# Kernel tuning notes

Hardware: AMD Instinct MI355X
Metric: run time of the kernel (lower is better)

The kernel has to match this reference:

```python
import jax, jax.numpy as jnp
import numpy as np

B, W, F = 64, 128, 64          # batch, window (node feat dim), n_features (nodes)
H, OUTW = 4, 128               # num_heads, out window size
NEG_SLOPE = 0.2                # LeakyReLU negative slope (alpha)


def setup_inputs() -> dict:
    key = jax.random.key(0)
    ks = jax.random.split(key, 6)
    scale_in = 1.0 / np.sqrt(W)
    scale_a = 1.0 / np.sqrt(OUTW)
    return {
        "x": jax.random.normal(ks[0], (B, W, F), dtype=jnp.float32),
        "W_src": jax.random.normal(ks[1], (H * OUTW, W), dtype=jnp.float32) * scale_in,
        "b_src": jnp.zeros((H * OUTW,), dtype=jnp.float32),
        "W_dst": jax.random.normal(ks[2], (H * OUTW, W), dtype=jnp.float32) * scale_in,
        "b_dst": jnp.zeros((H * OUTW,), dtype=jnp.float32),
        "attn": jax.random.normal(ks[3], (H, OUTW), dtype=jnp.float32) * scale_a,
    }


def reference(x, W_src, b_src, W_dst, b_dst, attn):
    # x: [B, W, F] -> node features nf: [B, F, W] (F nodes, W-dim features)
    nf = jnp.transpose(x, (0, 2, 1))
    b, f, w = nf.shape
    h, outw = attn.shape
    # GATv2 separate source/destination projections (share_weights=False)
    fs = (nf @ W_src.T + b_src).reshape(b, f, h, outw)  # [B, F, H, outW]
    fd = (nf @ W_dst.T + b_dst).reshape(b, f, h, outw)
    # additive score over complete graph with self-loops: e[b,i,j,h,d]
    s = fs[:, :, None, :, :] + fd[:, None, :, :, :]      # [B, src, dst, H, outW]
    e = jnp.where(s >= 0, s, NEG_SLOPE * s)              # LeakyReLU
    scores = jnp.einsum('bijhd,hd->bhij', e, attn)       # [B, H, src, dst]
    # edge softmax: normalize over incoming edges (sources) per destination
    a = jax.nn.softmax(scores, axis=2)
    # weighted scatter-sum aggregation at destinations
    out = jnp.einsum('bhij,bihd->bjhd', a, fs)           # [B, F, H, outW]
    out = out.mean(axis=2)                               # mean over heads -> [B, F, outW]
    return jnp.transpose(out, (0, 2, 1))                 # [B, outW, F]
```

## Files before the change

kernel.cpp:

```cpp
#include <hip/hip_runtime.h>
#include <math.h>

#define BB 64
#define WW 128
#define FF 64
#define HH 4
#define OW 128


struct GemmRegion {
    float xq[64 * 68];
    float wq[2 * 128 * 68];
};
struct AttnRegion {
    float fsl[FF * 132];
    float fdl[FF * 132];
    float st[FF * 68];
    float A6[OW], B4[OW];
    float redm[8 * 64];
    float reds[8 * 64];
};
union SMem { GemmRegion g; AttnRegion a; };

__global__ void __launch_bounds__(512)
__attribute__((amdgpu_waves_per_eu(2, 2)))
gat_fused(
    const float* __restrict__ x,
    const float* __restrict__ Wsrc,
    const float* __restrict__ bsrc,
    const float* __restrict__ Wdst,
    const float* __restrict__ bdst,
    const float* __restrict__ attn,
    float* __restrict__ out)
{
    __shared__ __align__(16) SMem sm;
    __shared__ float bl[2 * 128];

    const int bx = blockIdx.x;
    const int h  = bx & 3;
    const int b  = bx >> 2;
    const int t  = threadIdx.x;

    const int m  = t >> 7;
    const int ig = (t >> 4) & 7;
    const int dg = t & 15;
    const int i0 = ig * 8;

    if (t < 256) bl[t] = (t & 128 ? bdst : bsrc)[h * 128 + (t & 127)];

    float acc[8][8] = {};

    for (int kh = 0; kh < 2; ++kh) {
        if (kh) __syncthreads();
        #pragma unroll
        for (int p = 0; p < 2; ++p) {
            const int idx = p * 512 + t;
            const int k = idx >> 4, iq = idx & 15;
            *(float4*)&sm.g.xq[k * 68 + iq * 4] =
                *(const float4*)(x + ((size_t)b * WW + kh * 64 + k) * FF + iq * 4);
        }
        #pragma unroll
        for (int p = 0; p < 8; ++p) {
            const int idx = p * 512 + t;
            const int mm = idx >> 11, d = (idx >> 4) & 127, q = idx & 15;
            *(float4*)&sm.g.wq[(mm * 128 + d) * 68 + q * 4] =
                *(const float4*)((mm ? Wdst : Wsrc)
                                 + (size_t)(h * 128 + d) * WW + kh * 64 + q * 4);
        }
        __syncthreads();

        if (t < 256) {
            #pragma unroll 1
            for (int k0 = 0; k0 < 64; k0 += 4) {
                float4 wv[8];
                #pragma unroll
                for (int e = 0; e < 8; ++e)
                    wv[e] = *(const float4*)&sm.g.wq[(m * 128 + dg + 16 * e) * 68 + k0];
                #pragma unroll
                for (int kk = 0; kk < 4; ++kk) {
                    const float4 xa = *(const float4*)&sm.g.xq[(k0 + kk) * 68 + i0];
                    const float4 xb = *(const float4*)&sm.g.xq[(k0 + kk) * 68 + i0 + 4];
                    #pragma unroll
                    for (int e = 0; e < 8; ++e) {
                        const float wf = ((const float*)&wv[e])[kk];
                        acc[0][e] = fmaf(xa.x, wf, acc[0][e]);
                        acc[1][e] = fmaf(xa.y, wf, acc[1][e]);
                        acc[2][e] = fmaf(xa.z, wf, acc[2][e]);
                        acc[3][e] = fmaf(xa.w, wf, acc[3][e]);
                        acc[4][e] = fmaf(xb.x, wf, acc[4][e]);
                        acc[5][e] = fmaf(xb.y, wf, acc[5][e]);
                        acc[6][e] = fmaf(xb.z, wf, acc[6][e]);
                        acc[7][e] = fmaf(xb.w, wf, acc[7][e]);
                    }
                }
            }
        }
    }
    __syncthreads();

    if (t < 256) {
        float* dst = m ? sm.a.fdl : sm.a.fsl;
        #pragma unroll
        for (int e = 0; e < 8; ++e) {
            const int d = dg + 16 * e;
            const float bv = bl[m * 128 + d];
            #pragma unroll
            for (int ii = 0; ii < 8; ++ii)
                dst[(i0 + ii) * 132 + d] = acc[ii][e] + bv;
        }
    }
    if (t < 128) {
        const float av = attn[h * OW + t];
        sm.a.A6[t] = 0.6f * av;
        sm.a.B4[t] = 0.4f * av;
    }
    __syncthreads();

    if (t < 256) {
        const int i = t & 63, sel = t >> 6;
        const float* src = (sel < 2 ? sm.a.fsl : sm.a.fdl) + i * 132 + (sel & 1) * 64;
        const float* a6  = sm.a.A6 + (sel & 1) * 64;
        float s = 0.0f;
        #pragma unroll
        for (int c = 0; c < 16; ++c) {
            float4 fv = *(const float4*)&src[c * 4];
            float4 av = *(const float4*)&a6[c * 4];
            s = fmaf(fv.x, av.x, fmaf(fv.y, av.y, fmaf(fv.z, av.z, fmaf(fv.w, av.w, s))));
        }
        sm.a.redm[sel * 64 + i] = s;
    }
    __syncthreads();

    {
        const int lane = t & 63;
        const int jl0  = (t >> 6) * 8;
        float sc[8] = {};
        #pragma unroll 4
        for (int c = 0; c < 32; ++c) {
            const int dd0 = c * 4;
            float4 fsv = *(const float4*)&sm.a.fsl[lane * 132 + dd0];
            float4 b4  = *(const float4*)&sm.a.B4[dd0];
            #pragma unroll
            for (int jj = 0; jj < 8; ++jj) {
                float4 fdv = *(const float4*)&sm.a.fdl[(jl0 + jj) * 132 + dd0];
                float r = sc[jj];
                r = fmaf(b4.x, fabsf(fsv.x + fdv.x), r);
                r = fmaf(b4.y, fabsf(fsv.y + fdv.y), r);
                r = fmaf(b4.z, fabsf(fsv.z + fdv.z), r);
                r = fmaf(b4.w, fabsf(fsv.w + fdv.w), r);
                sc[jj] = r;
            }
        }
        const float csl = sm.a.redm[lane] + sm.a.redm[64 + lane];
        float4 o0, o1;
        o0.x = sc[0] + csl + sm.a.redm[128 + jl0 + 0] + sm.a.redm[192 + jl0 + 0];
        o0.y = sc[1] + csl + sm.a.redm[128 + jl0 + 1] + sm.a.redm[192 + jl0 + 1];
        o0.z = sc[2] + csl + sm.a.redm[128 + jl0 + 2] + sm.a.redm[192 + jl0 + 2];
        o0.w = sc[3] + csl + sm.a.redm[128 + jl0 + 3] + sm.a.redm[192 + jl0 + 3];
        o1.x = sc[4] + csl + sm.a.redm[128 + jl0 + 4] + sm.a.redm[192 + jl0 + 4];
        o1.y = sc[5] + csl + sm.a.redm[128 + jl0 + 5] + sm.a.redm[192 + jl0 + 5];
        o1.z = sc[6] + csl + sm.a.redm[128 + jl0 + 6] + sm.a.redm[192 + jl0 + 6];
        o1.w = sc[7] + csl + sm.a.redm[128 + jl0 + 7] + sm.a.redm[192 + jl0 + 7];
        *(float4*)&sm.a.st[lane * 68 + jl0]     = o0;
        *(float4*)&sm.a.st[lane * 68 + jl0 + 4] = o1;
    }
    __syncthreads();

    {
        const int j = t & 63, s = t >> 6;
        const int i0s = s * 8;
        float mx = sm.a.st[i0s * 68 + j];
        #pragma unroll
        for (int k = 1; k < 8; ++k) mx = fmaxf(mx, sm.a.st[(i0s + k) * 68 + j]);
        sm.a.redm[s * 64 + j] = mx;
    }
    __syncthreads();
    {
        const int j = t & 63, s = t >> 6;
        const int i0s = s * 8;
        float mj = sm.a.redm[j];
        #pragma unroll
        for (int s2 = 1; s2 < 8; ++s2) mj = fmaxf(mj, sm.a.redm[s2 * 64 + j]);
        float ps = 0.0f;
        #pragma unroll
        for (int k = 0; k < 8; ++k) {
            float e = __expf(sm.a.st[(i0s + k) * 68 + j] - mj);
            sm.a.st[(i0s + k) * 68 + j] = e;
            ps += e;
        }
        sm.a.reds[s * 64 + j] = ps;
    }
    __syncthreads();

    {
        const int j = t & 63, dblk = t >> 6;
        float l = 0.0f;
        #pragma unroll
        for (int s2 = 0; s2 < 8; ++s2) l += sm.a.reds[s2 * 64 + j];
        const float iv = 0.25f / l;

        float ag[16] = {};
        #pragma unroll 4
        for (int i = 0; i < FF; ++i) {
            const float p = sm.a.st[i * 68 + j];
            const float* fr = &sm.a.fsl[i * 132 + dblk * 16];
            float4 f0 = *(const float4*)(fr);
            float4 f1 = *(const float4*)(fr + 4);
            float4 f2 = *(const float4*)(fr + 8);
            float4 f3 = *(const float4*)(fr + 12);
            ag[0]  = fmaf(p, f0.x, ag[0]);  ag[1]  = fmaf(p, f0.y, ag[1]);
            ag[2]  = fmaf(p, f0.z, ag[2]);  ag[3]  = fmaf(p, f0.w, ag[3]);
            ag[4]  = fmaf(p, f1.x, ag[4]);  ag[5]  = fmaf(p, f1.y, ag[5]);
            ag[6]  = fmaf(p, f1.z, ag[6]);  ag[7]  = fmaf(p, f1.w, ag[7]);
            ag[8]  = fmaf(p, f2.x, ag[8]);  ag[9]  = fmaf(p, f2.y, ag[9]);
            ag[10] = fmaf(p, f2.z, ag[10]); ag[11] = fmaf(p, f2.w, ag[11]);
            ag[12] = fmaf(p, f3.x, ag[12]); ag[13] = fmaf(p, f3.y, ag[13]);
            ag[14] = fmaf(p, f3.z, ag[14]); ag[15] = fmaf(p, f3.w, ag[15]);
        }
        float* ob = out + ((size_t)b * OW + dblk * 16) * FF + j;
        #pragma unroll
        for (int e = 0; e < 16; ++e)
            atomicAdd(ob + e * FF, ag[e] * iv);
    }
}

extern "C" void kernel_launch(void* const* d_in, const int* in_sizes, int n_in,
                              void* d_out, int out_size, void* d_ws, size_t ws_size,
                              hipStream_t stream) {
    const float* x    = (const float*)d_in[0];
    const float* Wsrc = (const float*)d_in[1];
    const float* bsrc = (const float*)d_in[2];
    const float* Wdst = (const float*)d_in[3];
    const float* bdst = (const float*)d_in[4];
    const float* attn = (const float*)d_in[5];

    hipMemsetAsync(d_out, 0, (size_t)out_size, stream);
    gat_fused<<<BB * HH, 512, 0, stream>>>(x, Wsrc, bsrc, Wdst, bdst, attn,
                                           (float*)d_out);
}
```

Measured before the change: 105.2 us.

## Stream GEMM weights from global into registers and retile score and aggregation loops

```diff
diff --git a/kernel.cpp b/kernel.cpp
--- a/kernel.cpp
+++ b/kernel.cpp
@@ -10,12 +10,12 @@
 
 struct GemmRegion {
     float xq[64 * 68];
-    float wq[2 * 128 * 68];
 };
 struct AttnRegion {
     float fsl[FF * 132];
     float fdl[FF * 132];
     float st[FF * 68];
+    float st2[FF * 68];
     float A6[OW], B4[OW];
     float redm[8 * 64];
     float reds[8 * 64];
@@ -41,12 +41,14 @@
     const int b  = bx >> 2;
     const int t  = threadIdx.x;
 
-    const int m  = t >> 7;
+    const int m  = (t >> 7) & 1;
     const int ig = (t >> 4) & 7;
     const int dg = t & 15;
     const int i0 = ig * 8;
 
     if (t < 256) bl[t] = (t & 128 ? bdst : bsrc)[h * 128 + (t & 127)];
+
+    const float* wbase = (m ? Wdst : Wsrc) + (size_t)(h * 128 + dg) * WW;
 
     float acc[8][8] = {};
 
@@ -59,23 +61,22 @@
             *(float4*)&sm.g.xq[k * 68 + iq * 4] =
                 *(const float4*)(x + ((size_t)b * WW + kh * 64 + k) * FF + iq * 4);
         }
-        #pragma unroll
-        for (int p = 0; p < 8; ++p) {
-            const int idx = p * 512 + t;
-            const int mm = idx >> 11, d = (idx >> 4) & 127, q = idx & 15;
-            *(float4*)&sm.g.wq[(mm * 128 + d) * 68 + q * 4] =
-                *(const float4*)((mm ? Wdst : Wsrc)
-                                 + (size_t)(h * 128 + d) * WW + kh * 64 + q * 4);
-        }
         __syncthreads();
 
         if (t < 256) {
+            const float* wk = wbase + kh * 64;
+            float4 wv[8];
+            #pragma unroll
+            for (int e = 0; e < 8; ++e)
+                wv[e] = *(const float4*)(wk + (size_t)(16 * e) * WW);
             #pragma unroll 1
             for (int k0 = 0; k0 < 64; k0 += 4) {
-                float4 wv[8];
-                #pragma unroll
-                for (int e = 0; e < 8; ++e)
-                    wv[e] = *(const float4*)&sm.g.wq[(m * 128 + dg + 16 * e) * 68 + k0];
+                float4 wn[8];
+                if (k0 < 60) {
+                    #pragma unroll
+                    for (int e = 0; e < 8; ++e)
+                        wn[e] = *(const float4*)(wk + (size_t)(16 * e) * WW + k0 + 4);
+                }
                 #pragma unroll
                 for (int kk = 0; kk < 4; ++kk) {
                     const float4 xa = *(const float4*)&sm.g.xq[(k0 + kk) * 68 + i0];
@@ -93,6 +94,8 @@
                         acc[7][e] = fmaf(xb.w, wf, acc[7][e]);
                     }
                 }
+                #pragma unroll
+                for (int e = 0; e < 8; ++e) wv[e] = wn[e];
             }
         }
     }
@@ -132,37 +135,59 @@
     __syncthreads();
 
     {
-        const int lane = t & 63;
-        const int jl0  = (t >> 6) * 8;
-        float sc[8] = {};
+        const int dh  = t >> 8;
+        const int rem = t & 255;
+        const int i0D = (rem & 15) * 4;
+        const int j0D = (rem >> 4) * 4;
+        float4 scq[4];
+        scq[0] = scq[1] = scq[2] = scq[3] = float4{0.f, 0.f, 0.f, 0.f};
+        const int cBase = dh * 16;
         #pragma unroll 4
-        for (int c = 0; c < 32; ++c) {
-            const int dd0 = c * 4;
-            float4 fsv = *(const float4*)&sm.a.fsl[lane * 132 + dd0];
-            float4 b4  = *(const float4*)&sm.a.B4[dd0];
-            #pragma unroll
-            for (int jj = 0; jj < 8; ++jj) {
-                float4 fdv = *(const float4*)&sm.a.fdl[(jl0 + jj) * 132 + dd0];
-                float r = sc[jj];
-                r = fmaf(b4.x, fabsf(fsv.x + fdv.x), r);
-                r = fmaf(b4.y, fabsf(fsv.y + fdv.y), r);
-                r = fmaf(b4.z, fabsf(fsv.z + fdv.z), r);
-                r = fmaf(b4.w, fabsf(fsv.w + fdv.w), r);
-                sc[jj] = r;
-            }
-        }
-        const float csl = sm.a.redm[lane] + sm.a.redm[64 + lane];
-        float4 o0, o1;
-        o0.x = sc[0] + csl + sm.a.redm[128 + jl0 + 0] + sm.a.redm[192 + jl0 + 0];
-        o0.y = sc[1] + csl + sm.a.redm[128 + jl0 + 1] + sm.a.redm[192 + jl0 + 1];
-        o0.z = sc[2] + csl + sm.a.redm[128 + jl0 + 2] + sm.a.redm[192 + jl0 + 2];
-        o0.w = sc[3] + csl + sm.a.redm[128 + jl0 + 3] + sm.a.redm[192 + jl0 + 3];
-        o1.x = sc[4] + csl + sm.a.redm[128 + jl0 + 4] + sm.a.redm[192 + jl0 + 4];
-        o1.y = sc[5] + csl + sm.a.redm[128 + jl0 + 5] + sm.a.redm[192 + jl0 + 5];
-        o1.z = sc[6] + csl + sm.a.redm[128 + jl0 + 6] + sm.a.redm[192 + jl0 + 6];
-        o1.w = sc[7] + csl + sm.a.redm[128 + jl0 + 7] + sm.a.redm[192 + jl0 + 7];
-        *(float4*)&sm.a.st[lane * 68 + jl0]     = o0;
-        *(float4*)&sm.a.st[lane * 68 + jl0 + 4] = o1;
+        for (int c = 0; c < 16; ++c) {
+            const int dd0 = (cBase + c) * 4;
+            const float4 b4 = *(const float4*)&sm.a.B4[dd0];
+            float4 fdv[4];
+            #pragma unroll
+            for (int jj = 0; jj < 4; ++jj)
+                fdv[jj] = *(const float4*)&sm.a.fdl[(j0D + jj) * 132 + dd0];
+            #pragma unroll
+            for (int ii = 0; ii < 4; ++ii) {
+                const float4 fsv = *(const float4*)&sm.a.fsl[(i0D + ii) * 132 + dd0];
+                float* sc = (float*)&scq[ii];
+                #pragma unroll
+                for (int jj = 0; jj < 4; ++jj) {
+                    float r = sc[jj];
+                    r = fmaf(b4.x, fabsf(fsv.x + fdv[jj].x), r);
+                    r = fmaf(b4.y, fabsf(fsv.y + fdv[jj].y), r);
+                    r = fmaf(b4.z, fabsf(fsv.z + fdv[jj].z), r);
+                    r = fmaf(b4.w, fabsf(fsv.w + fdv[jj].w), r);
+                    sc[jj] = r;
+                }
+            }
+        }
+        if (dh) {
+            #pragma unroll
+            for (int ii = 0; ii < 4; ++ii)
+                *(float4*)&sm.a.st2[(i0D + ii) * 68 + j0D] = scq[ii];
+        }
+        __syncthreads();
+        if (!dh) {
+            float cdj[4];
+            #pragma unroll
+            for (int jj = 0; jj < 4; ++jj)
+                cdj[jj] = sm.a.redm[128 + j0D + jj] + sm.a.redm[192 + j0D + jj];
+            #pragma unroll
+            for (int ii = 0; ii < 4; ++ii) {
+                const float4 p2 = *(const float4*)&sm.a.st2[(i0D + ii) * 68 + j0D];
+                const float csl = sm.a.redm[i0D + ii] + sm.a.redm[64 + i0D + ii];
+                float4 o;
+                o.x = scq[ii].x + p2.x + csl + cdj[0];
+                o.y = scq[ii].y + p2.y + csl + cdj[1];
+                o.z = scq[ii].z + p2.z + csl + cdj[2];
+                o.w = scq[ii].w + p2.w + csl + cdj[3];
+                *(float4*)&sm.a.st[(i0D + ii) * 68 + j0D] = o;
+            }
+        }
     }
     __syncthreads();
 
@@ -193,34 +218,48 @@
     __syncthreads();
 
     {
-        const int j = t & 63, dblk = t >> 6;
-        float l = 0.0f;
-        #pragma unroll
-        for (int s2 = 0; s2 < 8; ++s2) l += sm.a.reds[s2 * 64 + j];
-        const float iv = 0.25f / l;
-
-        float ag[16] = {};
+        const int ih  = t >> 8;
+        const int rem = t & 255;
+        const int j0F = (rem & 15) * 4;
+        const int dF  = (rem >> 4) * 8;
+        float iv[4];
+        #pragma unroll
+        for (int jj = 0; jj < 4; ++jj) {
+            float l = 0.0f;
+            #pragma unroll
+            for (int s2 = 0; s2 < 8; ++s2) l += sm.a.reds[s2 * 64 + j0F + jj];
+            iv[jj] = 0.25f / l;
+        }
+        float ag[4][8] = {};
+        const int iBase = ih * 32;
         #pragma unroll 4
-        for (int i = 0; i < FF; ++i) {
-            const float p = sm.a.st[i * 68 + j];
-            const float* fr = &sm.a.fsl[i * 132 + dblk * 16];
-            float4 f0 = *(const float4*)(fr);
-            float4 f1 = *(const float4*)(fr + 4);
-            float4 f2 = *(const float4*)(fr + 8);
-            float4 f3 = *(const float4*)(fr + 12);
-            ag[0]  = fmaf(p, f0.x, ag[0]);  ag[1]  = fmaf(p, f0.y, ag[1]);
-            ag[2]  = fmaf(p, f0.z, ag[2]);  ag[3]  = fmaf(p, f0.w, ag[3]);
-            ag[4]  = fmaf(p, f1.x, ag[4]);  ag[5]  = fmaf(p, f1.y, ag[5]);
-            ag[6]  = fmaf(p, f1.z, ag[6]);  ag[7]  = fmaf(p, f1.w, ag[7]);
-            ag[8]  = fmaf(p, f2.x, ag[8]);  ag[9]  = fmaf(p, f2.y, ag[9]);
-            ag[10] = fmaf(p, f2.z, ag[10]); ag[11] = fmaf(p, f2.w, ag[11]);
-            ag[12] = fmaf(p, f3.x, ag[12]); ag[13] = fmaf(p, f3.y, ag[13]);
-            ag[14] = fmaf(p, f3.z, ag[14]); ag[15] = fmaf(p, f3.w, ag[15]);
-        }
-        float* ob = out + ((size_t)b * OW + dblk * 16) * FF + j;
-        #pragma unroll
-        for (int e = 0; e < 16; ++e)
-            atomicAdd(ob + e * FF, ag[e] * iv);
+        for (int i2 = 0; i2 < 32; ++i2) {
+            const int i = iBase + i2;
+            const float4 pv = *(const float4*)&sm.a.st[i * 68 + j0F];
+            const float* fr = &sm.a.fsl[i * 132 + dF];
+            const float4 f0 = *(const float4*)(fr);
+            const float4 f1 = *(const float4*)(fr + 4);
+            const float* pp = (const float*)&pv;
+            #pragma unroll
+            for (int jj = 0; jj < 4; ++jj) {
+                const float p = pp[jj];
+                ag[jj][0] = fmaf(p, f0.x, ag[jj][0]);
+                ag[jj][1] = fmaf(p, f0.y, ag[jj][1]);
+                ag[jj][2] = fmaf(p, f0.z, ag[jj][2]);
+                ag[jj][3] = fmaf(p, f0.w, ag[jj][3]);
+                ag[jj][4] = fmaf(p, f1.x, ag[jj][4]);
+                ag[jj][5] = fmaf(p, f1.y, ag[jj][5]);
+                ag[jj][6] = fmaf(p, f1.z, ag[jj][6]);
+                ag[jj][7] = fmaf(p, f1.w, ag[jj][7]);
+            }
+        }
+        float* ob = out + ((size_t)b * OW + dF) * FF;
+        #pragma unroll
+        for (int jj = 0; jj < 4; ++jj) {
+            #pragma unroll
+            for (int dd = 0; dd < 8; ++dd)
+                atomicAdd(ob + (size_t)dd * FF + j0F + jj, ag[jj][dd] * iv[jj]);
+        }
     }
 }
 
```

Result: slower. 159.0 us (+51.2%).
